# Optimization experiments

Measured on AMD Instinct MI355X. Metric: run time of the kernel, lower is better.

The kernel has to match this reference:

```python
import jax, jax.numpy as jnp
import numpy as np

N, D = 4096, 128
NUM_CLASS = 500000
NUM_SAMPLES = 32768


def setup_inputs() -> dict:
    key = jax.random.key(0)
    k_x, k_w, k_b, k_id = jax.random.split(key, 4)
    x = jax.random.normal(k_x, (N, D), dtype=jnp.float32)
    # params.weight init uniform(-0.05, 0.05) in original; use randn-scaled equivalent scale
    weight = jax.random.normal(k_w, (NUM_CLASS, D), dtype=jnp.float32) * 0.05
    bias = jax.random.normal(k_b, (NUM_CLASS, 1), dtype=jnp.float32) * 0.01
    # sample_ids: candidate classes returned by the LSH hash-table query (host-side
    # data structure); modeled here as a precomputed index set.
    sample_ids = jax.random.randint(k_id, (NUM_SAMPLES,), 0, NUM_CLASS, dtype=jnp.int64)
    return {"x": x, "weight": weight, "bias": bias, "sample_ids": sample_ids}


def reference(x, weight, bias, sample_ids):
    # gather sampled class embeddings + biases (F.embedding equivalent)
    sample_weights = weight[sample_ids]            # [S, D]
    sample_bias = bias[:, 0][sample_ids]           # [S]
    # small GEMM: [N, D] @ [D, S] + [S]
    sample_logits = jnp.einsum("nd,sd->ns", x, sample_weights) + sample_bias
    return (sample_logits, sample_ids)
```

## Files before the change

### kernel.cpp

```cpp
#include <hip/hip_runtime.h>
#include <hip/hip_bf16.h>

#define NROWS 4096
#define DIM   128
#define SCOLS 32768

typedef short bf16x8 __attribute__((ext_vector_type(8)));
typedef float f32x4  __attribute__((ext_vector_type(4)));

__device__ __forceinline__ unsigned short f2bf(float f) {
    unsigned int u = __builtin_bit_cast(unsigned int, f);
    u += 0x7fffu + ((u >> 16) & 1u);
    return (unsigned short)(u >> 16);
}

__global__ __launch_bounds__(256, 2) void lsh_gemm(
    const float* __restrict__ x,
    const float* __restrict__ weight,
    const float* __restrict__ bias,
    const int*   __restrict__ ids,
    float*       __restrict__ out)
{
    __shared__ unsigned short lds_x[128 * 128];
    __shared__ unsigned short lds_w[128 * 128];

    const int t  = threadIdx.x;
    const int s0 = blockIdx.x * 128;
    const int n0 = blockIdx.y * 128;

    #pragma unroll
    for (int i = 0; i < 16; ++i) {
        int f   = t + i * 256;
        int row = f >> 5;
        int c4  = f & 31;
        float4 v = ((const float4*)(x + (size_t)(n0 + row) * DIM))[c4];
        ushort4 b;
        b.x = f2bf(v.x); b.y = f2bf(v.y); b.z = f2bf(v.z); b.w = f2bf(v.w);
        int sw = (c4 >> 1) ^ (row & 15);
        *(ushort4*)&lds_x[row * 128 + sw * 8 + (c4 & 1) * 4] = b;
    }
    #pragma unroll
    for (int i = 0; i < 16; ++i) {
        int f   = t + i * 256;
        int row = f >> 5;
        int c4  = f & 31;
        int id  = ids[s0 + row];
        float4 v = ((const float4*)(weight + (size_t)id * DIM))[c4];
        ushort4 b;
        b.x = f2bf(v.x); b.y = f2bf(v.y); b.z = f2bf(v.z); b.w = f2bf(v.w);
        int sw = (c4 >> 1) ^ (row & 15);
        *(ushort4*)&lds_w[row * 128 + sw * 8 + (c4 & 1) * 4] = b;
    }
    __syncthreads();

    const int lane = t & 63;
    const int wave = t >> 6;
    const int lrow = lane & 15;
    const int quad = lane >> 4;
    const int wm   = (wave & 1) * 64;
    const int wsc  = (wave >> 1) * 64;

    f32x4 acc[4][4];
    #pragma unroll
    for (int a = 0; a < 4; ++a)
        #pragma unroll
        for (int b = 0; b < 4; ++b)
            acc[a][b] = (f32x4){0.f, 0.f, 0.f, 0.f};

    #pragma unroll
    for (int kk = 0; kk < 4; ++kk) {
        bf16x8 af[4], bv[4];
        int cbase = kk * 4 + quad;
        #pragma unroll
        for (int i = 0; i < 4; ++i) {
            int rowa = wm  + i * 16 + lrow;
            int rowb = wsc + i * 16 + lrow;
            af[i] = *(const bf16x8*)&lds_x[rowa * 128 + (cbase ^ lrow) * 8];
            bv[i] = *(const bf16x8*)&lds_w[rowb * 128 + (cbase ^ lrow) * 8];
        }
        #pragma unroll
        for (int tm = 0; tm < 4; ++tm)
            #pragma unroll
            for (int ts = 0; ts < 4; ++ts)
                acc[tm][ts] = __builtin_amdgcn_mfma_f32_16x16x32_bf16(
                    af[tm], bv[ts], acc[tm][ts], 0, 0, 0);
    }

    #pragma unroll
    for (int ts = 0; ts < 4; ++ts) {
        int colL = wsc + ts * 16 + lrow;
        int col  = s0 + colL;
        float bvps = bias[ids[s0 + colL]];
        #pragma unroll
        for (int tm = 0; tm < 4; ++tm) {
            int rowbase = n0 + wm + tm * 16 + quad * 4;
            #pragma unroll
            for (int r = 0; r < 4; ++r)
                out[(size_t)(rowbase + r) * SCOLS + col] = acc[tm][ts][r] + bvps;
        }
    }
}

__global__ void ids_out_kernel(const int* __restrict__ ids, float* __restrict__ out)
{
    int i = blockIdx.x * 256 + threadIdx.x;
    if (i < SCOLS)
        out[(size_t)NROWS * SCOLS + i] = (float)ids[i];
}

extern "C" void kernel_launch(void* const* d_in, const int* in_sizes, int n_in,
                              void* d_out, int out_size, void* d_ws, size_t ws_size,
                              hipStream_t stream) {
    const float* x      = (const float*)d_in[0];
    const float* weight = (const float*)d_in[1];
    const float* bias   = (const float*)d_in[2];
    const int*   ids    = (const int*)d_in[3];
    float*       out    = (float*)d_out;

    hipLaunchKernelGGL(lsh_gemm, dim3(SCOLS / 128, NROWS / 128), dim3(256), 0, stream,
                       x, weight, bias, ids, out);
    hipLaunchKernelGGL(ids_out_kernel, dim3(SCOLS / 256), dim3(256), 0, stream,
                       ids, out);
}
```

Before: 737.2 us.

## Pre-gather and convert operands to bf16 workspace, load via direct-to-LDS

Adds a prep kernel that gathers the sampled weight rows, converts weight and x to pre-swizzled bf16 in a workspace, gathers biases and writes the ids output. The GEMM kernel then fills LDS with global_load_lds and no per-thread conversion, swaps operand roles so each lane stores contiguous float4 outputs with nontemporal stores, and reads bias as a vector. This removes the repeated gather and fp32-to-bf16 conversion, which the old code redid for every row tile, and makes the dominant output writes wider. The cost is an extra kernel launch and a workspace round trip; the old path remains as a fallback when the workspace is too small.

Measured after the change: 660.7 us. -10.4%, faster.

```diff
diff --git a/kernel.cpp b/kernel.cpp
--- a/kernel.cpp
+++ b/kernel.cpp
@@ -1,5 +1,4 @@
 #include <hip/hip_runtime.h>
-#include <hip/hip_bf16.h>
 
 #define NROWS 4096
 #define DIM   128
@@ -12,6 +11,121 @@
     unsigned int u = __builtin_bit_cast(unsigned int, f);
     u += 0x7fffu + ((u >> 16) & 1u);
     return (unsigned short)(u >> 16);
+}
+
+#define WCHUNKS (SCOLS * 16)
+#define XCHUNKS (NROWS * 16)
+
+__global__ __launch_bounds__(256) void prep_kernel(
+    const float* __restrict__ x, const float* __restrict__ weight,
+    const float* __restrict__ bias, const int* __restrict__ ids,
+    float* __restrict__ out, unsigned short* __restrict__ w_ws,
+    unsigned short* __restrict__ x_ws, float* __restrict__ bias_ws)
+{
+    int gid = blockIdx.x * 256 + threadIdx.x;
+    if (gid < WCHUNKS) {
+        int r = gid >> 4, c = gid & 15;
+        int id = ids[r];
+        const float4* src = (const float4*)(weight + (size_t)id * DIM);
+        float4 v0 = src[2 * c], v1 = src[2 * c + 1];
+        union { unsigned short u[8]; uint4 q; } b;
+        b.u[0] = f2bf(v0.x); b.u[1] = f2bf(v0.y); b.u[2] = f2bf(v0.z); b.u[3] = f2bf(v0.w);
+        b.u[4] = f2bf(v1.x); b.u[5] = f2bf(v1.y); b.u[6] = f2bf(v1.z); b.u[7] = f2bf(v1.w);
+        *(uint4*)&w_ws[(size_t)r * DIM + (size_t)((c ^ (r & 15)) * 8)] = b.q;
+    } else if (gid < WCHUNKS + XCHUNKS) {
+        int g = gid - WCHUNKS;
+        int r = g >> 4, c = g & 15;
+        const float4* src = (const float4*)(x + (size_t)r * DIM);
+        float4 v0 = src[2 * c], v1 = src[2 * c + 1];
+        union { unsigned short u[8]; uint4 q; } b;
+        b.u[0] = f2bf(v0.x); b.u[1] = f2bf(v0.y); b.u[2] = f2bf(v0.z); b.u[3] = f2bf(v0.w);
+        b.u[4] = f2bf(v1.x); b.u[5] = f2bf(v1.y); b.u[6] = f2bf(v1.z); b.u[7] = f2bf(v1.w);
+        *(uint4*)&x_ws[(size_t)r * DIM + (size_t)((c ^ (r & 15)) * 8)] = b.q;
+    } else {
+        int g = gid - (WCHUNKS + XCHUNKS);
+        if (g < SCOLS) {
+            int id = ids[g];
+            bias_ws[g] = bias[id];
+            out[(size_t)NROWS * SCOLS + g] = (float)id;
+        }
+    }
+}
+
+__global__ __launch_bounds__(256, 2) void lsh_gemm2(
+    const unsigned short* __restrict__ w_ws,
+    const unsigned short* __restrict__ x_ws,
+    const float* __restrict__ bias_ws,
+    float* __restrict__ out)
+{
+    __shared__ unsigned short lds_w[128 * 128];
+    __shared__ unsigned short lds_x[128 * 128];
+
+    const int t    = threadIdx.x;
+    const int s0   = blockIdx.x * 128;
+    const int n0   = blockIdx.y * 128;
+    const int lane = t & 63;
+    const int wave = t >> 6;
+
+    const char* wsrc = (const char*)(w_ws + (size_t)s0 * DIM);
+    const char* xsrc = (const char*)(x_ws + (size_t)n0 * DIM);
+
+    #pragma unroll
+    for (int j = 0; j < 8; ++j) {
+        int boff = wave * 8192 + j * 1024;
+        int goff = boff + lane * 16;
+        __builtin_amdgcn_global_load_lds(
+            (const __attribute__((address_space(1))) void*)(wsrc + goff),
+            (__attribute__((address_space(3))) void*)((char*)lds_w + boff),
+            16, 0, 0);
+        __builtin_amdgcn_global_load_lds(
+            (const __attribute__((address_space(1))) void*)(xsrc + goff),
+            (__attribute__((address_space(3))) void*)((char*)lds_x + boff),
+            16, 0, 0);
+    }
+    __syncthreads();
+
+    const int lrow = lane & 15;
+    const int quad = lane >> 4;
+    const int wn   = (wave & 1) * 64;
+    const int wsc  = (wave >> 1) * 64;
+
+    f32x4 acc[4][4];
+    #pragma unroll
+    for (int a = 0; a < 4; ++a)
+        #pragma unroll
+        for (int b = 0; b < 4; ++b)
+            acc[a][b] = (f32x4){0.f, 0.f, 0.f, 0.f};
+
+    #pragma unroll
+    for (int kk = 0; kk < 4; ++kk) {
+        bf16x8 aw[4], bx[4];
+        int cb = kk * 4 + quad;
+        #pragma unroll
+        for (int i = 0; i < 4; ++i) {
+            int rw = wsc + i * 16 + lrow;
+            int rn = wn  + i * 16 + lrow;
+            aw[i] = *(const bf16x8*)&lds_w[rw * 128 + ((cb ^ lrow) * 8)];
+            bx[i] = *(const bf16x8*)&lds_x[rn * 128 + ((cb ^ lrow) * 8)];
+        }
+        #pragma unroll
+        for (int a = 0; a < 4; ++a)
+            #pragma unroll
+            for (int b = 0; b < 4; ++b)
+                acc[a][b] = __builtin_amdgcn_mfma_f32_16x16x32_bf16(
+                    aw[a], bx[b], acc[a][b], 0, 0, 0);
+    }
+
+    #pragma unroll
+    for (int a = 0; a < 4; ++a) {
+        int sL = wsc + a * 16 + quad * 4;
+        f32x4 b4 = *(const f32x4*)&bias_ws[s0 + sL];
+        #pragma unroll
+        for (int b = 0; b < 4; ++b) {
+            int n = n0 + wn + b * 16 + lrow;
+            f32x4 v = acc[a][b] + b4;
+            __builtin_nontemporal_store(v, (f32x4*)&out[(size_t)n * SCOLS + (s0 + sL)]);
+        }
+    }
 }
 
 __global__ __launch_bounds__(256, 2) void lsh_gemm(
@@ -117,8 +231,24 @@
     const int*   ids    = (const int*)d_in[3];
     float*       out    = (float*)d_out;
 
-    hipLaunchKernelGGL(lsh_gemm, dim3(SCOLS / 128, NROWS / 128), dim3(256), 0, stream,
-                       x, weight, bias, ids, out);
-    hipLaunchKernelGGL(ids_out_kernel, dim3(SCOLS / 256), dim3(256), 0, stream,
-                       ids, out);
-}
+    const size_t W_BYTES = (size_t)SCOLS * DIM * 2;
+    const size_t X_BYTES = (size_t)NROWS * DIM * 2;
+    const size_t B_BYTES = (size_t)SCOLS * 4;
+
+    if (ws_size >= W_BYTES + X_BYTES + B_BYTES) {
+        unsigned short* w_ws   = (unsigned short*)d_ws;
+        unsigned short* x_ws   = (unsigned short*)((char*)d_ws + W_BYTES);
+        float*          bias_ws = (float*)((char*)d_ws + W_BYTES + X_BYTES);
+
+        const int prep_blocks = (WCHUNKS + XCHUNKS + SCOLS) / 256;
+        hipLaunchKernelGGL(prep_kernel, dim3(prep_blocks), dim3(256), 0, stream,
+                           x, weight, bias, ids, out, w_ws, x_ws, bias_ws);
+        hipLaunchKernelGGL(lsh_gemm2, dim3(SCOLS / 128, NROWS / 128), dim3(256), 0, stream,
+                           w_ws, x_ws, bias_ws, out);
+    } else {
+        hipLaunchKernelGGL(lsh_gemm, dim3(SCOLS / 128, NROWS / 128), dim3(256), 0, stream,
+                           x, weight, bias, ids, out);
+        hipLaunchKernelGGL(ids_out_kernel, dim3(SCOLS / 256), dim3(256), 0, stream,
+                           ids, out);
+    }
+}
```
